# Kernel optimization log

Hardware: AMD Instinct MI355X
Metric: run time of the kernel (lower is better)

## Reference

```python
import jax, jax.numpy as jnp
import numpy as np

N_DIFFS = 8388608
N_BINS = 100
N_CAP = 2


def setup_inputs() -> dict:
    key = jax.random.key(0)
    k1, k2 = jax.random.split(key)
    bin_centers = jax.random.uniform(k1, (N_BINS,), dtype=jnp.float32)
    obs_probs_idxs = jax.random.randint(k2, (N_DIFFS, N_CAP), 0, N_BINS)
    return {
        "bin_centers": bin_centers,
        "obs_probs_idxs": obs_probs_idxs,
        "pre_beta": 4.0 * jnp.ones((N_CAP,), jnp.float32),
        "pre_can_l": -10.0 * jnp.ones((N_CAP,), jnp.float32),
        "pre_can_u": 10.0 * jnp.ones((N_CAP,), jnp.float32),
        "pre_will_l": -10.0 * jnp.ones((1,), jnp.float32),
        "pre_will_u": 10.0 * jnp.ones((1,), jnp.float32),
    }


def reference(bin_centers, obs_probs_idxs, pre_beta, pre_can_l, pre_can_u, pre_will_l, pre_will_u):
    # Swap-if-out-of-order (original mutates params in place; equivalent to min/max)
    cl_raw = jnp.minimum(pre_can_l, pre_can_u)
    cu_raw = jnp.maximum(pre_can_l, pre_can_u)
    wl_raw = jnp.minimum(pre_will_l, pre_will_u)
    wu_raw = jnp.maximum(pre_will_l, pre_will_u)

    can_l = jax.nn.sigmoid(cl_raw)   # [n_cap]
    can_u = jax.nn.sigmoid(cu_raw)   # [n_cap]
    will = 0.5 * (jax.nn.sigmoid(wl_raw) + jax.nn.sigmoid(wu_raw))[0]  # scalar
    beta = pre_beta * pre_beta       # [n_cap]

    p = bin_centers[obs_probs_idxs]  # [n_diffs, n_cap], gather

    denom = can_u - can_l            # [n_cap], broadcast over rows
    # smooth branch: 1 - 1/(b*(cu-cl)) * log((1+e^{b(p-cl)})/(1+e^{b(p-cu)}))
    smooth = 1.0 - (1.0 / (beta * denom)) * (
        jnp.log1p(jnp.exp(beta * (p - can_l))) - jnp.log1p(jnp.exp(beta * (p - can_u)))
    )
    linear = (can_u - p) / (denom + 1e-4)
    trust_temp = jnp.where(
        beta < -50.0,
        smooth,
        jnp.where(p <= can_l, 1.0, jnp.where(p > can_u, 0.0, linear)),
    )  # [n_diffs, n_cap]

    trust = jnp.prod(trust_temp, axis=1) * will  # [n_diffs]
    return trust
```

## Files before the change

### kernel.cpp

```cpp
#include <hip/hip_runtime.h>
#include <math.h>

#define N_BINS 100
#define N_CAP  2

__device__ __forceinline__ float sigmoidf(float x) {
    return 1.0f / (1.0f + expf(-x));
}

__global__ __launch_bounds__(256) void RobotTrustModel_trust_kernel(
        const float* __restrict__ bin_centers,
        const float* __restrict__ pre_beta,
        const float* __restrict__ pre_can_l,
        const float* __restrict__ pre_can_u,
        const float* __restrict__ pre_will_l,
        const float* __restrict__ pre_will_u,
        const int4*  __restrict__ idx,
        float2*      __restrict__ out,
        int n_pairs) {
    __shared__ float slut[N_CAP * N_BINS];

    int tid    = threadIdx.x;
    int gid    = blockIdx.x * blockDim.x + tid;
    int stride = gridDim.x * blockDim.x;

    int  t = gid;
    int4 v = make_int4(0, 0, 0, 0);
    if (t < n_pairs) v = idx[t];

    if (tid < N_CAP * N_BINS) {
        int cap = tid / N_BINS;
        int bin = tid % N_BINS;

        float cl_raw = fminf(pre_can_l[cap], pre_can_u[cap]);
        float cu_raw = fmaxf(pre_can_l[cap], pre_can_u[cap]);
        float can_l = sigmoidf(cl_raw);
        float can_u = sigmoidf(cu_raw);

        float wl_raw = fminf(pre_will_l[0], pre_will_u[0]);
        float wu_raw = fmaxf(pre_will_l[0], pre_will_u[0]);
        float will = 0.5f * (sigmoidf(wl_raw) + sigmoidf(wu_raw));

        float beta  = pre_beta[cap] * pre_beta[cap];
        float denom = can_u - can_l;
        float p     = bin_centers[bin];

        float tt;
        if (beta < -50.0f) {
            tt = 1.0f - (1.0f / (beta * denom)) *
                 (log1pf(expf(beta * (p - can_l))) - log1pf(expf(beta * (p - can_u))));
        } else {
            tt = (p <= can_l) ? 1.0f
               : ((p > can_u) ? 0.0f
               : (can_u - p) / (denom + 1e-4f));
        }
        if (cap == 0) tt *= will;
        slut[cap * N_BINS + bin] = tt;
    }
    __syncthreads();

    while (t < n_pairs) {
        int  tn = t + stride;
        int4 vn = make_int4(0, 0, 0, 0);
        if (tn < n_pairs) vn = idx[tn];

        float2 a;
        a.x = slut[v.x] * slut[N_BINS + v.y];
        a.y = slut[v.z] * slut[N_BINS + v.w];
        out[t] = a;

        v = vn;
        t = tn;
    }
}

extern "C" void kernel_launch(void* const* d_in, const int* in_sizes, int n_in,
                              void* d_out, int out_size, void* d_ws, size_t ws_size,
                              hipStream_t stream) {
    const float* bin_centers = (const float*)d_in[0];
    const int*   obs_idx     = (const int*)d_in[1];
    const float* pre_beta    = (const float*)d_in[2];
    const float* pre_can_l   = (const float*)d_in[3];
    const float* pre_can_u   = (const float*)d_in[4];
    const float* pre_will_l  = (const float*)d_in[5];
    const float* pre_will_u  = (const float*)d_in[6];

    float* out = (float*)d_out;

    int n_diffs = in_sizes[1] / N_CAP;
    int n_pairs = n_diffs / 2;

    int block = 256;
    int grid  = 4096;
    RobotTrustModel_trust_kernel<<<grid, block, 0, stream>>>(
        bin_centers, pre_beta, pre_can_l, pre_can_u, pre_will_l, pre_will_u,
        (const int4*)obs_idx, (float2*)out, n_pairs);
}
```

Before: 21.17 us.

## Replace grid-stride loop with one-shot threads handling four outputs each

Drops the persistent grid-stride loop with software prefetch and launches enough blocks to cover all outputs, each thread loading two int4 index vectors and writing a float4. This widens the stores and removes loop overhead. The cost is that every block now rebuilds the shared lookup table, which adds sigmoid/exp work and a barrier per block, and cross-iteration load prefetching is gone.

```diff
diff --git a/kernel.cpp b/kernel.cpp
--- a/kernel.cpp
+++ b/kernel.cpp
@@ -16,17 +16,18 @@
         const float* __restrict__ pre_will_l,
         const float* __restrict__ pre_will_u,
         const int4*  __restrict__ idx,
-        float2*      __restrict__ out,
-        int n_pairs) {
+        float4*      __restrict__ out,
+        int n_quads) {
     __shared__ float slut[N_CAP * N_BINS];
 
-    int tid    = threadIdx.x;
-    int gid    = blockIdx.x * blockDim.x + tid;
-    int stride = gridDim.x * blockDim.x;
+    int tid = threadIdx.x;
+    int t   = blockIdx.x * blockDim.x + tid;
 
-    int  t = gid;
-    int4 v = make_int4(0, 0, 0, 0);
-    if (t < n_pairs) v = idx[t];
+    int4 v0 = make_int4(0, 0, 0, 0), v1 = make_int4(0, 0, 0, 0);
+    if (t < n_quads) {
+        v0 = idx[2 * t];
+        v1 = idx[2 * t + 1];
+    }
 
     if (tid < N_CAP * N_BINS) {
         int cap = tid / N_BINS;
@@ -59,18 +60,13 @@
     }
     __syncthreads();
 
-    while (t < n_pairs) {
-        int  tn = t + stride;
-        int4 vn = make_int4(0, 0, 0, 0);
-        if (tn < n_pairs) vn = idx[tn];
-
-        float2 a;
-        a.x = slut[v.x] * slut[N_BINS + v.y];
-        a.y = slut[v.z] * slut[N_BINS + v.w];
-        out[t] = a;
-
-        v = vn;
-        t = tn;
+    if (t < n_quads) {
+        float4 r;
+        r.x = slut[v0.x] * slut[N_BINS + v0.y];
+        r.y = slut[v0.z] * slut[N_BINS + v0.w];
+        r.z = slut[v1.x] * slut[N_BINS + v1.y];
+        r.w = slut[v1.z] * slut[N_BINS + v1.w];
+        out[t] = r;
     }
 }
 
@@ -88,11 +84,11 @@
     float* out = (float*)d_out;
 
     int n_diffs = in_sizes[1] / N_CAP;
-    int n_pairs = n_diffs / 2;
+    int n_quads = n_diffs / 4;
+    int block   = 256;
+    int grid    = (n_quads + block - 1) / block;
 
-    int block = 256;
-    int grid  = 4096;
     RobotTrustModel_trust_kernel<<<grid, block, 0, stream>>>(
         bin_centers, pre_beta, pre_can_l, pre_can_u, pre_will_l, pre_will_u,
-        (const int4*)obs_idx, (float2*)out, n_pairs);
+        (const int4*)obs_idx, (float4*)out, n_quads);
 }
```

New measurement: 20.81 us, median of 2. Within noise of the previous version (-1.7%).
